# Kernel optimization log

Hardware: AMD Instinct MI355X
Metric: run time of the kernel (lower is better)

Reference implementation:

```python
import jax, jax.numpy as jnp
import numpy as np

S = 128           # seq_len
B = 256           # input_bits (bits per token, also neurons per head)
H = 16            # num_heads
NB = 12           # n_bits_per_neuron -> LUT size 2^12
PB = 7            # relative-position bits = ceil(log2(max_seq_len))
HEAD_IN = 2 * B + PB   # concat(query, key, rel_pos_bits) = 519
THRESH = H // 2


def setup_inputs() -> dict:
    key = jax.random.key(0)
    k1, k2, k3 = jax.random.split(key, 3)
    tokens = jax.random.randint(k1, (S, B), 0, 2, dtype=jnp.int32)           # binary token bits
    memory = jax.random.normal(k2, (H, B, 2 ** NB), dtype=jnp.float32)       # RAM LUT contents per head/neuron
    connections = jax.random.randint(k3, (H, B, NB), 0, HEAD_IN, dtype=jnp.int32)  # per-neuron input-bit wiring
    return {"tokens": tokens, "memory": memory, "connections": connections}


def reference(tokens, memory, connections):
    idx = jnp.arange(S)
    rel = idx[:, None] - idx[None, :]                         # [S,S] i - j
    mask = (rel >= 0).astype(jnp.int32)                        # causal mask (j <= i)
    relc = jnp.clip(rel, 0, S - 1)
    # relative-distance binary encoding, LSB first: [S,S,PB]
    pos_bits = ((relc[..., None] >> jnp.arange(PB)) & 1).astype(jnp.int32)
    q = jnp.broadcast_to(tokens[:, None, :], (S, S, B))
    k = jnp.broadcast_to(tokens[None, :, :], (S, S, B))
    head_in = jnp.concatenate([q, k, pos_bits], axis=-1)       # [S,S,HEAD_IN]
    # RAM address per (query i, key j, head h, neuron n): pack NB wired bits, LSB first
    addr = jnp.zeros((S, S, H, B), dtype=jnp.int32)
    for b in range(NB):  # tiny fixed loop over bit planes, fully vectorized over S,S,H,B
        addr = addr + (head_in[..., connections[:, :, b]] << b)
    # LUT gather: memory[h, n, addr] -> [S,S,H,B]
    h_idx = jnp.arange(H)[:, None]
    n_idx = jnp.arange(B)[None, :]
    vals = memory[h_idx, n_idx, addr]
    bits = (vals > 0.0).astype(jnp.int32)                      # RAM neuron output bit
    # XOR accumulation over attended keys == masked sum mod 2: [S,H,B]
    head_res = jnp.sum(bits * mask[:, :, None, None], axis=1) % 2
    # majority vote across heads per bit
    ones_count = jnp.sum(head_res, axis=1)                     # [S,B]
    return (ones_count > THRESH).astype(jnp.int32)
```

## Files before the change

### kernel.cpp

```cpp
#include <hip/hip_runtime.h>


#define S 128
#define B 256
#define H 16
#define NB 12

__device__ __forceinline__ unsigned sig(unsigned x) {
    return x ^ ((x >> 3) & 0x70u) ^ ((x >> 6) & 0x70u);
}

#define TW(c) ((((c) & 3) << 1) + ((c) >> 7))
#define TP(c) (((c) >> 2) & 31)

__global__ __launch_bounds__(256) void pack_kernel(
    const int* __restrict__ tokens,
    unsigned* __restrict__ tokP)
{
    const int wid  = threadIdx.x >> 6;
    const int lane = threadIdx.x & 63;
    const int4* tp = (const int4*)tokens;
    #pragma unroll
    for (int r = 0; r < 4; ++r) {
        int i = blockIdx.x * 16 + wid * 4 + r;
        int4 x = tp[i * 64 + lane];
        unsigned long long B0 = __ballot((x.x & 1) != 0);
        unsigned long long B1 = __ballot((x.y & 1) != 0);
        unsigned long long B2 = __ballot((x.z & 1) != 0);
        unsigned long long B3 = __ballot((x.w & 1) != 0);
        int c = lane >> 1;
        unsigned long long s01 = (c & 1) ? B1 : B0;
        unsigned long long s23 = (c & 1) ? B3 : B2;
        unsigned long long s   = (c & 2) ? s23 : s01;
        unsigned word = (lane & 1) ? (unsigned)(s >> 32) : (unsigned)s;
        if (lane < 8) tokP[lane * 128 + i] = word;
    }
}

__global__ __launch_bounds__(256, 4) void softram_kernel(
    const unsigned* __restrict__ tokP,
    const float* __restrict__ memory,
    const int* __restrict__ connections,
    unsigned char* __restrict__ pc)
{
    const int bid  = blockIdx.x;
    const int g    = bid >> 8;
    const int n    = bid & 255;
    const int tid  = threadIdx.x;
    const int wid  = tid >> 6;
    const int hg   = g * 4 + wid;
    const int lane = tid & 63;

    __shared__ __align__(16) unsigned char  bytetab[4 * 4096];
    __shared__ __align__(16) unsigned int   tokT[8 * S];
    __shared__ __align__(16) unsigned short akT[4][S];
    __shared__ __align__(16) unsigned short apt[4][S];
    __shared__ int            conns[4][NB];
    __shared__ unsigned int   parts[4][4];

    const float4* mrow = (const float4*)(memory + ((size_t)(hg * 256 + n) << 12));
    float4 va[16];
    #pragma unroll
    for (int t = 0; t < 16; ++t) va[t] = mrow[lane + 64 * t];

    ((int4*)tokT)[tid] = ((const int4*)tokP)[tid];
    if (tid < 4 * NB) {
        int hh = tid / NB, b = tid - hh * NB;
        conns[hh][b] = connections[(size_t)(g * 4 + hh) * (B * NB) + n * NB + b];
    }
    __syncthreads();

    unsigned qmask = 0, kmask = 0, pmask = 0;
    #pragma unroll
    for (int b = 0; b < NB; ++b) {
        int c = conns[wid][b];
        qmask |= (unsigned)(c < 256) << b;
        kmask |= (unsigned)(c >= 256 && c < 512) << b;
        pmask |= (unsigned)(c >= 512) << b;
    }
    const int qb = __popc(qmask);
    const int kb = __popc(kmask);

    unsigned char* __restrict__ bt = &bytetab[wid << 12];
    unsigned long long rlo = 0, rhi = 0;

    if (pmask == 0) {
        unsigned qclsA = 0, qclsB = 0;
        #pragma unroll
        for (int e = 0; e < 2; ++e) {
            int ii = lane + 64 * e;
            unsigned qc = 0, kc = 0;
            int qn = 0, kn = 0;
            #pragma unroll
            for (int b = 0; b < NB; ++b) {
                int c = conns[wid][b];
                if (c < 256) {
                    qc |= ((tokT[TW(c) * S + ii] >> TP(c)) & 1u) << qn;
                    ++qn;
                } else {
                    int c2 = c - 256;
                    kc |= ((tokT[TW(c2) * S + ii] >> TP(c2)) & 1u) << kn;
                    ++kn;
                }
            }
            akT[wid][ii] = (unsigned short)kc;
            if (e == 0) qclsA = qc; else qclsB = qc;
        }

        #pragma unroll
        for (int t = 0; t < 16; ++t) {
            float4 v = va[t];
            unsigned p = 4u * (unsigned)(lane + 64 * t);
            unsigned w = (unsigned)(v.x > 0.f)
                       | ((unsigned)(v.y > 0.f) << 8)
                       | ((unsigned)(v.z > 0.f) << 16)
                       | ((unsigned)(v.w > 0.f) << 24);
            *(unsigned*)&bt[sig(p)] = w;
        }

        const bool formA = (qb <= 6);
        const int SBITS  = formA ? qb : kb;
        unsigned apl = 0, aul = 0;
        {
            int scnt = 0, lcnt = 0;
            #pragma unroll
            for (int b = 0; b < NB; ++b) {
                int c = conns[wid][b];
                bool isS = formA ? (c < 256) : (c >= 256);
                if (isS) {
                    apl |= (((unsigned)lane >> scnt) & 1u) << b;
                    ++scnt;
                } else {
                    int p = SBITS + lcnt;
                    if (p < 6) apl |= (((unsigned)lane >> p) & 1u) << b;
                    else       aul |= (((unsigned)lane >> (p - 6)) & 1u) << b;
                    ++lcnt;
                }
            }
        }
        const unsigned spl  = sig(apl);
        const unsigned saul = sig(aul);
        unsigned Wlo = 0, Whi = 0;
        #pragma unroll 8
        for (int it = 0; it < 64; ++it) {
            unsigned sau  = (unsigned)__builtin_amdgcn_readlane((int)saul, it);
            unsigned bitv = bt[sau ^ spl] & 1u;
            unsigned long long Bm = __ballot(bitv != 0u);
#if __has_builtin(__builtin_amdgcn_writelane)
            Wlo = (unsigned)__builtin_amdgcn_writelane((int)(unsigned)Bm, it, (int)Wlo);
            Whi = (unsigned)__builtin_amdgcn_writelane((int)(unsigned)(Bm >> 32), it, (int)Whi);
#else
            Wlo = (lane == it) ? (unsigned)Bm : Wlo;
            Whi = (lane == it) ? (unsigned)(Bm >> 32) : Whi;
#endif
        }
        const unsigned long long Wfull = ((unsigned long long)Whi << 32) | Wlo;

        if (formA) {
            unsigned kclsA = akT[wid][lane];
            unsigned g0 = kclsA << qb;
            unsigned long long V = __shfl(Wfull, (int)(g0 >> 6)) >> (g0 & 63u);
            #pragma unroll
            for (int d = 1; d < 64; d <<= 1) {
                unsigned long long u = __shfl_up(V, (unsigned)d);
                V ^= (lane >= d) ? u : 0ull;
            }
            rlo = __ballot(((V >> qclsA) & 1ull) != 0ull);
            const unsigned long long Abase = __shfl(V, 63);

            unsigned kclsB = akT[wid][64 + lane];
            unsigned g1 = kclsB << qb;
            unsigned long long V1 = __shfl(Wfull, (int)(g1 >> 6)) >> (g1 & 63u);
            #pragma unroll
            for (int d = 1; d < 64; d <<= 1) {
                unsigned long long u = __shfl_up(V1, (unsigned)d);
                V1 ^= (lane >= d) ? u : 0ull;
            }
            V1 ^= Abase;
            rhi = __ballot(((V1 >> qclsB) & 1ull) != 0ull);
        } else {
            unsigned kclsA = akT[wid][lane];
            unsigned C = 1u << kclsA;
            #pragma unroll
            for (int d = 1; d < 64; d <<= 1) {
                unsigned u = __shfl_up(C, (unsigned)d);
                C ^= (lane >= d) ? u : 0u;
            }
            unsigned g0a = qclsA << kb;
            unsigned W0 = (unsigned)(__shfl(Wfull, (int)(g0a >> 6)) >> (g0a & 63u));
            rlo = __ballot((__popc(W0 & C) & 1) != 0);
            const unsigned Cbase = __shfl(C, 63);

            unsigned kclsB = akT[wid][64 + lane];
            unsigned C1 = 1u << kclsB;
            #pragma unroll
            for (int d = 1; d < 64; d <<= 1) {
                unsigned u = __shfl_up(C1, (unsigned)d);
                C1 ^= (lane >= d) ? u : 0u;
            }
            C1 ^= Cbase;
            unsigned g0b = qclsB << kb;
            unsigned W1 = (unsigned)(__shfl(Wfull, (int)(g0b >> 6)) >> (g0b & 63u));
            rhi = __ballot((__popc(W1 & C1) & 1) != 0);
        }
    } else {
        unsigned aqv0 = 0, aqv1 = 0;
        #pragma unroll
        for (int e = 0; e < 2; ++e) {
            int ii = lane + 64 * e;
            unsigned aq = 0, ak = 0, ap = 0;
            #pragma unroll
            for (int b = 0; b < NB; ++b) {
                int c = conns[wid][b];
                if (c < 256) {
                    aq |= ((tokT[TW(c) * S + ii] >> TP(c)) & 1u) << b;
                } else if (c < 512) {
                    int c2 = c - 256;
                    ak |= ((tokT[TW(c2) * S + ii] >> TP(c2)) & 1u) << b;
                } else {
                    ap |= (((unsigned)ii >> (c - 512)) & 1u) << b;
                }
            }
            akT[wid][ii] = (unsigned short)sig(ak);
            apt[wid][ii] = (unsigned short)sig(ap);
            if (e == 0) aqv0 = sig(aq); else aqv1 = sig(aq);
        }

        #pragma unroll
        for (int t = 0; t < 16; ++t) {
            float4 v = va[t];
            unsigned p = 4u * (unsigned)(lane + 64 * t);
            unsigned w = (unsigned)(v.x > 0.f)
                       | ((unsigned)(v.y > 0.f) << 8)
                       | ((unsigned)(v.z > 0.f) << 16)
                       | ((unsigned)(v.w > 0.f) << 24);
            *(unsigned*)&bt[sig(p)] = w;
        }

        unsigned acc0 = 0, acc1 = 0;
        for (int s8 = 0; s8 < 8; ++s8) {
            uint4 uk = *(const uint4*)&akT[wid][s8 * 8];
            #pragma unroll
            for (int t = 0; t < 8; ++t) {
                int j = s8 * 8 + t;
                unsigned w = ((const unsigned*)&uk)[t >> 1];
                unsigned akv = (w >> ((t & 1) * 16)) & 0xffffu;
                int d0 = lane - j;
                unsigned v0 = bt[aqv0 ^ akv ^ (unsigned)apt[wid][d0 & 127]] & 1u;
                acc0 ^= (d0 >= 0) ? v0 : 0u;
                int d1 = lane + 64 - j;
                unsigned v1 = bt[aqv1 ^ akv ^ (unsigned)apt[wid][d1]] & 1u;
                acc1 ^= v1;
            }
        }
        for (int s8 = 8; s8 < 16; ++s8) {
            uint4 uk = *(const uint4*)&akT[wid][s8 * 8];
            #pragma unroll
            for (int t = 0; t < 8; ++t) {
                int j = s8 * 8 + t;
                unsigned w = ((const unsigned*)&uk)[t >> 1];
                unsigned akv = (w >> ((t & 1) * 16)) & 0xffffu;
                int d1 = lane + 64 - j;
                unsigned v1 = bt[aqv1 ^ akv ^ (unsigned)apt[wid][d1 & 127]] & 1u;
                acc1 ^= (d1 >= 0) ? v1 : 0u;
            }
        }
        rlo = __ballot(acc0 != 0u);
        rhi = __ballot(acc1 != 0u);
    }

    if (lane == 0) {
        parts[wid][0] = (unsigned)rlo;
        parts[wid][1] = (unsigned)(rlo >> 32);
        parts[wid][2] = (unsigned)rhi;
        parts[wid][3] = (unsigned)(rhi >> 32);
    }
    __syncthreads();

    if (tid < S) {
        int i = tid, tot = 0;
        #pragma unroll
        for (int hh = 0; hh < 4; ++hh)
            tot += (parts[hh][i >> 5] >> (i & 31)) & 1;
        pc[((size_t)g * 256 + n) * 128 + i] = (unsigned char)tot;
    }
}

__global__ __launch_bounds__(128) void vote_kernel(
    const unsigned char* __restrict__ pc,
    int* __restrict__ out)
{
    const int n = blockIdx.x;
    const int i = threadIdx.x;
    int tot = pc[(size_t)(0 * 256 + n) * 128 + i]
            + pc[(size_t)(1 * 256 + n) * 128 + i]
            + pc[(size_t)(2 * 256 + n) * 128 + i]
            + pc[(size_t)(3 * 256 + n) * 128 + i];
    out[i * B + n] = (tot > (H / 2)) ? 1 : 0;
}

extern "C" void kernel_launch(void* const* d_in, const int* in_sizes, int n_in,
                              void* d_out, int out_size, void* d_ws, size_t ws_size,
                              hipStream_t stream) {
    const int*   tokens      = (const int*)d_in[0];
    const float* memory      = (const float*)d_in[1];
    const int*   connections = (const int*)d_in[2];
    int*         out         = (int*)d_out;
    unsigned char* pc        = (unsigned char*)d_ws;
    unsigned*      tokP      = (unsigned*)((char*)d_ws + 4 * 256 * 128);
    (void)in_sizes; (void)n_in; (void)out_size; (void)ws_size;

    pack_kernel<<<8, 256, 0, stream>>>(tokens, tokP);
    softram_kernel<<<4 * B, 256, 0, stream>>>(tokP, memory, connections, pc);
    vote_kernel<<<B, 128, 0, stream>>>(pc, out);
}
```

Measured before the change: 110.0 us.

## Stream LUT rows through LDS with async global_load_lds pipeline

Replaces the 16 register-held float4 loads of each neuron's LUT row with direct global-to-LDS async loads into a 4-slot staging ring, consumed step by step with explicit vmcnt waits. Each step refills its slot four chunks ahead. The address computation for both branches is moved ahead of the staging loop so it overlaps the memory latency. The aim is to cut VGPR pressure (64 registers for va) and raise occupancy while keeping loads in flight. In exchange it uses 16KB more LDS per block, which may itself limit occupancy, and relies on hand-written waitcnt ordering.

After: 110.4 us. About the same (+0.4%).

```diff
diff --git a/kernel.cpp b/kernel.cpp
--- a/kernel.cpp
+++ b/kernel.cpp
@@ -52,16 +52,16 @@
     const int lane = tid & 63;
 
     __shared__ __align__(16) unsigned char  bytetab[4 * 4096];
+    __shared__ __align__(16) float          stage[4][4 * 256];
     __shared__ __align__(16) unsigned int   tokT[8 * S];
     __shared__ __align__(16) unsigned short akT[4][S];
     __shared__ __align__(16) unsigned short apt[4][S];
     __shared__ int            conns[4][NB];
     __shared__ unsigned int   parts[4][4];
 
-    const float4* mrow = (const float4*)(memory + ((size_t)(hg * 256 + n) << 12));
-    float4 va[16];
-    #pragma unroll
-    for (int t = 0; t < 16; ++t) va[t] = mrow[lane + 64 * t];
+    const float* gbase = memory + ((size_t)(hg * 256 + n) << 12);
+    float*       sbase = &stage[wid][0];
+    unsigned char* __restrict__ bt = &bytetab[wid << 12];
 
     ((int4*)tokT)[tid] = ((const int4*)tokP)[tid];
     if (tid < 4 * NB) {
@@ -69,6 +69,16 @@
         conns[hh][b] = connections[(size_t)(g * 4 + hh) * (B * NB) + n * NB + b];
     }
     __syncthreads();
+
+#if __has_builtin(__builtin_amdgcn_global_load_lds)
+#define GLLD(T) __builtin_amdgcn_global_load_lds( \
+        (const __attribute__((address_space(1))) void*)(gbase + (T) * 256 + lane * 4), \
+        (__attribute__((address_space(3))) void*)(sbase + ((T) & 3) * 256), 16, 0, 0)
+#else
+#define GLLD(T) do { *(float4*)(sbase + ((T) & 3) * 256 + lane * 4) = \
+        *(const float4*)(gbase + (T) * 256 + lane * 4); } while (0)
+#endif
+    GLLD(0); GLLD(1); GLLD(2); GLLD(3);
 
     unsigned qmask = 0, kmask = 0, pmask = 0;
     #pragma unroll
@@ -80,12 +90,10 @@
     }
     const int qb = __popc(qmask);
     const int kb = __popc(kmask);
-
-    unsigned char* __restrict__ bt = &bytetab[wid << 12];
-    unsigned long long rlo = 0, rhi = 0;
-
-    if (pmask == 0) {
-        unsigned qclsA = 0, qclsB = 0;
+    const bool fast = (pmask == 0);
+
+    unsigned qclsA = 0, qclsB = 0;
+    if (fast) {
         #pragma unroll
         for (int e = 0; e < 2; ++e) {
             int ii = lane + 64 * e;
@@ -106,18 +114,52 @@
             akT[wid][ii] = (unsigned short)kc;
             if (e == 0) qclsA = qc; else qclsB = qc;
         }
-
+    } else {
         #pragma unroll
-        for (int t = 0; t < 16; ++t) {
-            float4 v = va[t];
-            unsigned p = 4u * (unsigned)(lane + 64 * t);
-            unsigned w = (unsigned)(v.x > 0.f)
-                       | ((unsigned)(v.y > 0.f) << 8)
-                       | ((unsigned)(v.z > 0.f) << 16)
-                       | ((unsigned)(v.w > 0.f) << 24);
-            *(unsigned*)&bt[sig(p)] = w;
-        }
-
+        for (int e = 0; e < 2; ++e) {
+            int ii = lane + 64 * e;
+            unsigned aq = 0, ak = 0, ap = 0;
+            #pragma unroll
+            for (int b = 0; b < NB; ++b) {
+                int c = conns[wid][b];
+                if (c < 256) {
+                    aq |= ((tokT[TW(c) * S + ii] >> TP(c)) & 1u) << b;
+                } else if (c < 512) {
+                    int c2 = c - 256;
+                    ak |= ((tokT[TW(c2) * S + ii] >> TP(c2)) & 1u) << b;
+                } else {
+                    ap |= (((unsigned)ii >> (c - 512)) & 1u) << b;
+                }
+            }
+            akT[wid][ii] = (unsigned short)sig(ak);
+            apt[wid][ii] = (unsigned short)sig(ap);
+            if (e == 0) qclsA = sig(aq); else qclsB = sig(aq);
+        }
+    }
+
+#define STEP(T, NW) do { \
+    asm volatile("s_waitcnt vmcnt(" #NW ")" ::: "memory"); \
+    __builtin_amdgcn_sched_barrier(0); \
+    float4 v = *(const float4*)(sbase + ((T) & 3) * 256 + lane * 4); \
+    unsigned w = (unsigned)(v.x > 0.f) \
+               | ((unsigned)(v.y > 0.f) << 8) \
+               | ((unsigned)(v.z > 0.f) << 16) \
+               | ((unsigned)(v.w > 0.f) << 24); \
+    asm volatile("s_waitcnt lgkmcnt(0)" ::: "memory"); \
+    __builtin_amdgcn_sched_barrier(0); \
+    if ((T) + 4 < 16) { GLLD((T) + 4); } \
+    *(unsigned*)&bt[sig(4u * (unsigned)(lane + 64 * (T)))] = w; \
+} while (0)
+
+    STEP(0, 3);  STEP(1, 3);  STEP(2, 3);  STEP(3, 3);
+    STEP(4, 3);  STEP(5, 3);  STEP(6, 3);  STEP(7, 3);
+    STEP(8, 3);  STEP(9, 3);  STEP(10, 3); STEP(11, 3);
+    STEP(12, 3); STEP(13, 2); STEP(14, 1); STEP(15, 0);
+#undef STEP
+
+    unsigned long long rlo = 0, rhi = 0;
+
+    if (fast) {
         const bool formA = (qb <= 6);
         const int SBITS  = formA ? qb : kb;
         unsigned apl = 0, aul = 0;
@@ -204,39 +246,7 @@
             rhi = __ballot((__popc(W1 & C1) & 1) != 0);
         }
     } else {
-        unsigned aqv0 = 0, aqv1 = 0;
-        #pragma unroll
-        for (int e = 0; e < 2; ++e) {
-            int ii = lane + 64 * e;
-            unsigned aq = 0, ak = 0, ap = 0;
-            #pragma unroll
-            for (int b = 0; b < NB; ++b) {
-                int c = conns[wid][b];
-                if (c < 256) {
-                    aq |= ((tokT[TW(c) * S + ii] >> TP(c)) & 1u) << b;
-                } else if (c < 512) {
-                    int c2 = c - 256;
-                    ak |= ((tokT[TW(c2) * S + ii] >> TP(c2)) & 1u) << b;
-                } else {
-                    ap |= (((unsigned)ii >> (c - 512)) & 1u) << b;
-                }
-            }
-            akT[wid][ii] = (unsigned short)sig(ak);
-            apt[wid][ii] = (unsigned short)sig(ap);
-            if (e == 0) aqv0 = sig(aq); else aqv1 = sig(aq);
-        }
-
-        #pragma unroll
-        for (int t = 0; t < 16; ++t) {
-            float4 v = va[t];
-            unsigned p = 4u * (unsigned)(lane + 64 * t);
-            unsigned w = (unsigned)(v.x > 0.f)
-                       | ((unsigned)(v.y > 0.f) << 8)
-                       | ((unsigned)(v.z > 0.f) << 16)
-                       | ((unsigned)(v.w > 0.f) << 24);
-            *(unsigned*)&bt[sig(p)] = w;
-        }
-
+        const unsigned aqv0 = qclsA, aqv1 = qclsB;
         unsigned acc0 = 0, acc1 = 0;
         for (int s8 = 0; s8 < 8; ++s8) {
             uint4 uk = *(const uint4*)&akT[wid][s8 * 8];
```

## Move LUT thresholding and W-matrix construction into a separate prep kernel

Applied to the files above, without the earlier changes.

Splits the work so a new prep kernel reads the float LUT memory, thresholds it into a byte table, and for neurons with no position bits also builds the 64x64 bit matrix W, which goes to workspace. The main kernel then loads either the precomputed W (fast path) or the precomputed byte table, the latter via global-to-LDS loads. The goal is to take the large memory read and 16-float4 register array out of the main kernel to ease register pressure and shorten its critical path. In exchange it adds an extra global write/read round trip through workspace (up to 16 MB of byte tables), though the memory read itself is spread over more blocks.

After: 118.0 us. 7.3% more time.

```diff
diff --git a/kernel.cpp b/kernel.cpp
--- a/kernel.cpp
+++ b/kernel.cpp
@@ -13,34 +13,119 @@
 #define TW(c) ((((c) & 3) << 1) + ((c) >> 7))
 #define TP(c) (((c) >> 2) & 31)
 
-__global__ __launch_bounds__(256) void pack_kernel(
+__global__ __launch_bounds__(256, 4) void prep_kernel(
     const int* __restrict__ tokens,
-    unsigned* __restrict__ tokP)
+    const float* __restrict__ memory,
+    const int* __restrict__ connections,
+    unsigned* __restrict__ tokP,
+    unsigned long long* __restrict__ psW,
+    unsigned char* __restrict__ psB)
 {
     const int wid  = threadIdx.x >> 6;
     const int lane = threadIdx.x & 63;
-    const int4* tp = (const int4*)tokens;
+
+    if (blockIdx.x >= 1024) {
+        const int bid2 = blockIdx.x - 1024;
+        const int4* tp = (const int4*)tokens;
+        #pragma unroll
+        for (int rr = 0; rr < 4; ++rr) {
+            int i = bid2 * 16 + wid * 4 + rr;
+            int4 x = tp[i * 64 + lane];
+            unsigned long long B0 = __ballot((x.x & 1) != 0);
+            unsigned long long B1 = __ballot((x.y & 1) != 0);
+            unsigned long long B2 = __ballot((x.z & 1) != 0);
+            unsigned long long B3 = __ballot((x.w & 1) != 0);
+            int c = lane >> 1;
+            unsigned long long s01 = (c & 1) ? B1 : B0;
+            unsigned long long s23 = (c & 1) ? B3 : B2;
+            unsigned long long s   = (c & 2) ? s23 : s01;
+            unsigned word = (lane & 1) ? (unsigned)(s >> 32) : (unsigned)s;
+            if (lane < 8) tokP[lane * 128 + i] = word;
+        }
+        return;
+    }
+
+    __shared__ __align__(16) unsigned char bytetab[4][4096];
+    const int r = blockIdx.x * 4 + wid;
+    unsigned char* __restrict__ bt = bytetab[wid];
+
+    int c_l = (lane < NB) ? connections[(size_t)r * NB + lane] : 0;
+    unsigned qmask = 0, kmask = 0, pmask = 0;
     #pragma unroll
-    for (int r = 0; r < 4; ++r) {
-        int i = blockIdx.x * 16 + wid * 4 + r;
-        int4 x = tp[i * 64 + lane];
-        unsigned long long B0 = __ballot((x.x & 1) != 0);
-        unsigned long long B1 = __ballot((x.y & 1) != 0);
-        unsigned long long B2 = __ballot((x.z & 1) != 0);
-        unsigned long long B3 = __ballot((x.w & 1) != 0);
-        int c = lane >> 1;
-        unsigned long long s01 = (c & 1) ? B1 : B0;
-        unsigned long long s23 = (c & 1) ? B3 : B2;
-        unsigned long long s   = (c & 2) ? s23 : s01;
-        unsigned word = (lane & 1) ? (unsigned)(s >> 32) : (unsigned)s;
-        if (lane < 8) tokP[lane * 128 + i] = word;
-    }
+    for (int b = 0; b < NB; ++b) {
+        int cb = __shfl(c_l, b);
+        qmask |= (unsigned)(cb < 256) << b;
+        kmask |= (unsigned)(cb >= 256 && cb < 512) << b;
+        pmask |= (unsigned)(cb >= 512) << b;
+    }
+    const int qb = __popc(qmask);
+    const int kb = __popc(kmask);
+    const bool fast = (pmask == 0);
+
+    const float4* mp = (const float4*)(memory + ((size_t)r << 12));
+    unsigned char* __restrict__ gb = psB + ((size_t)r << 12);
+    float4 va[4];
+    #pragma unroll
+    for (int t = 0; t < 4; ++t) va[t] = mp[lane + 64 * t];
+    #pragma unroll
+    for (int t = 0; t < 16; ++t) {
+        float4 v = va[t & 3];
+        if (t + 4 < 16) va[t & 3] = mp[lane + 64 * (t + 4)];
+        unsigned w = (unsigned)(v.x > 0.f)
+                   | ((unsigned)(v.y > 0.f) << 8)
+                   | ((unsigned)(v.z > 0.f) << 16)
+                   | ((unsigned)(v.w > 0.f) << 24);
+        unsigned sp = sig(4u * (unsigned)(lane + 64 * t));
+        *(unsigned*)&bt[sp] = w;
+        if (!fast) *(unsigned*)&gb[sp] = w;
+    }
+
+    if (!fast) return;
+
+    const bool formA = (qb <= 6);
+    const int SBITS  = formA ? qb : kb;
+    unsigned apl = 0, aul = 0;
+    {
+        int scnt = 0, lcnt = 0;
+        #pragma unroll
+        for (int b = 0; b < NB; ++b) {
+            int cb = __shfl(c_l, b);
+            bool isS = formA ? (cb < 256) : (cb >= 256);
+            if (isS) {
+                apl |= (((unsigned)lane >> scnt) & 1u) << b;
+                ++scnt;
+            } else {
+                int p = SBITS + lcnt;
+                if (p < 6) apl |= (((unsigned)lane >> p) & 1u) << b;
+                else       aul |= (((unsigned)lane >> (p - 6)) & 1u) << b;
+                ++lcnt;
+            }
+        }
+    }
+    const unsigned spl  = sig(apl);
+    const unsigned saul = sig(aul);
+    unsigned Wlo = 0, Whi = 0;
+    #pragma unroll 8
+    for (int it = 0; it < 64; ++it) {
+        unsigned sau  = (unsigned)__builtin_amdgcn_readlane((int)saul, it);
+        unsigned bitv = bt[sau ^ spl] & 1u;
+        unsigned long long Bm = __ballot(bitv != 0u);
+#if __has_builtin(__builtin_amdgcn_writelane)
+        Wlo = (unsigned)__builtin_amdgcn_writelane((int)(unsigned)Bm, it, (int)Wlo);
+        Whi = (unsigned)__builtin_amdgcn_writelane((int)(unsigned)(Bm >> 32), it, (int)Whi);
+#else
+        Wlo = (lane == it) ? (unsigned)Bm : Wlo;
+        Whi = (lane == it) ? (unsigned)(Bm >> 32) : Whi;
+#endif
+    }
+    psW[(size_t)r * 64 + lane] = ((unsigned long long)Whi << 32) | Wlo;
 }
 
 __global__ __launch_bounds__(256, 4) void softram_kernel(
     const unsigned* __restrict__ tokP,
-    const float* __restrict__ memory,
     const int* __restrict__ connections,
+    const unsigned long long* __restrict__ psW,
+    const unsigned char* __restrict__ psB,
     unsigned char* __restrict__ pc)
 {
     const int bid  = blockIdx.x;
@@ -49,19 +134,17 @@
     const int tid  = threadIdx.x;
     const int wid  = tid >> 6;
     const int hg   = g * 4 + wid;
+    const int r    = hg * 256 + n;
     const int lane = tid & 63;
 
-    __shared__ __align__(16) unsigned char  bytetab[4 * 4096];
+    __shared__ __align__(16) unsigned char  bytetab[4][4096];
     __shared__ __align__(16) unsigned int   tokT[8 * S];
     __shared__ __align__(16) unsigned short akT[4][S];
     __shared__ __align__(16) unsigned short apt[4][S];
     __shared__ int            conns[4][NB];
     __shared__ unsigned int   parts[4][4];
 
-    const float4* mrow = (const float4*)(memory + ((size_t)(hg * 256 + n) << 12));
-    float4 va[16];
-    #pragma unroll
-    for (int t = 0; t < 16; ++t) va[t] = mrow[lane + 64 * t];
+    unsigned char* __restrict__ bt = bytetab[wid];
 
     ((int4*)tokT)[tid] = ((const int4*)tokP)[tid];
     if (tid < 4 * NB) {
@@ -80,11 +163,13 @@
     }
     const int qb = __popc(qmask);
     const int kb = __popc(kmask);
-
-    unsigned char* __restrict__ bt = &bytetab[wid << 12];
+    const bool fast = (pmask == 0);
+
     unsigned long long rlo = 0, rhi = 0;
 
-    if (pmask == 0) {
+    if (fast) {
+        const unsigned long long Wfull = psW[(size_t)r * 64 + lane];
+
         unsigned qclsA = 0, qclsB = 0;
         #pragma unroll
         for (int e = 0; e < 2; ++e) {
@@ -107,56 +192,7 @@
             if (e == 0) qclsA = qc; else qclsB = qc;
         }
 
-        #pragma unroll
-        for (int t = 0; t < 16; ++t) {
-            float4 v = va[t];
-            unsigned p = 4u * (unsigned)(lane + 64 * t);
-            unsigned w = (unsigned)(v.x > 0.f)
-                       | ((unsigned)(v.y > 0.f) << 8)
-                       | ((unsigned)(v.z > 0.f) << 16)
-                       | ((unsigned)(v.w > 0.f) << 24);
-            *(unsigned*)&bt[sig(p)] = w;
-        }
-
-        const bool formA = (qb <= 6);
-        const int SBITS  = formA ? qb : kb;
-        unsigned apl = 0, aul = 0;
-        {
-            int scnt = 0, lcnt = 0;
-            #pragma unroll
-            for (int b = 0; b < NB; ++b) {
-                int c = conns[wid][b];
-                bool isS = formA ? (c < 256) : (c >= 256);
-                if (isS) {
-                    apl |= (((unsigned)lane >> scnt) & 1u) << b;
-                    ++scnt;
-                } else {
-                    int p = SBITS + lcnt;
-                    if (p < 6) apl |= (((unsigned)lane >> p) & 1u) << b;
-                    else       aul |= (((unsigned)lane >> (p - 6)) & 1u) << b;
-                    ++lcnt;
-                }
-            }
-        }
-        const unsigned spl  = sig(apl);
-        const unsigned saul = sig(aul);
-        unsigned Wlo = 0, Whi = 0;
-        #pragma unroll 8
-        for (int it = 0; it < 64; ++it) {
-            unsigned sau  = (unsigned)__builtin_amdgcn_readlane((int)saul, it);
-            unsigned bitv = bt[sau ^ spl] & 1u;
-            unsigned long long Bm = __ballot(bitv != 0u);
-#if __has_builtin(__builtin_amdgcn_writelane)
-            Wlo = (unsigned)__builtin_amdgcn_writelane((int)(unsigned)Bm, it, (int)Wlo);
-            Whi = (unsigned)__builtin_amdgcn_writelane((int)(unsigned)(Bm >> 32), it, (int)Whi);
-#else
-            Wlo = (lane == it) ? (unsigned)Bm : Wlo;
-            Whi = (lane == it) ? (unsigned)(Bm >> 32) : Whi;
-#endif
-        }
-        const unsigned long long Wfull = ((unsigned long long)Whi << 32) | Wlo;
-
-        if (formA) {
+        if (qb <= 6) {
             unsigned kclsA = akT[wid][lane];
             unsigned g0 = kclsA << qb;
             unsigned long long V = __shfl(Wfull, (int)(g0 >> 6)) >> (g0 & 63u);
@@ -204,6 +240,21 @@
             rhi = __ballot((__popc(W1 & C1) & 1) != 0);
         }
     } else {
+        const unsigned char* __restrict__ gb = psB + ((size_t)r << 12);
+#if __has_builtin(__builtin_amdgcn_global_load_lds)
+        #pragma unroll
+        for (int t = 0; t < 4; ++t)
+            __builtin_amdgcn_global_load_lds(
+                (const __attribute__((address_space(1))) void*)(gb + t * 1024 + lane * 16),
+                (__attribute__((address_space(3))) void*)(bt + t * 1024 + lane * 16),
+                16, 0, 0);
+#else
+        #pragma unroll
+        for (int t = 0; t < 4; ++t)
+            *(float4*)(bt + t * 1024 + lane * 16) =
+                *(const float4*)(gb + t * 1024 + lane * 16);
+#endif
+
         unsigned aqv0 = 0, aqv1 = 0;
         #pragma unroll
         for (int e = 0; e < 2; ++e) {
@@ -226,16 +277,8 @@
             if (e == 0) aqv0 = sig(aq); else aqv1 = sig(aq);
         }
 
-        #pragma unroll
-        for (int t = 0; t < 16; ++t) {
-            float4 v = va[t];
-            unsigned p = 4u * (unsigned)(lane + 64 * t);
-            unsigned w = (unsigned)(v.x > 0.f)
-                       | ((unsigned)(v.y > 0.f) << 8)
-                       | ((unsigned)(v.z > 0.f) << 16)
-                       | ((unsigned)(v.w > 0.f) << 24);
-            *(unsigned*)&bt[sig(p)] = w;
-        }
+        asm volatile("s_waitcnt vmcnt(0)" ::: "memory");
+        __builtin_amdgcn_sched_barrier(0);
 
         unsigned acc0 = 0, acc1 = 0;
         for (int s8 = 0; s8 < 8; ++s8) {
@@ -306,11 +349,13 @@
     const float* memory      = (const float*)d_in[1];
     const int*   connections = (const int*)d_in[2];
     int*         out         = (int*)d_out;
-    unsigned char* pc        = (unsigned char*)d_ws;
-    unsigned*      tokP      = (unsigned*)((char*)d_ws + 4 * 256 * 128);
+    unsigned char*      pc   = (unsigned char*)d_ws;
+    unsigned*           tokP = (unsigned*)((char*)d_ws + (128u << 10));
+    unsigned long long* psW  = (unsigned long long*)((char*)d_ws + (1u << 20));
+    unsigned char*      psB  = (unsigned char*)d_ws + (4u << 20);
     (void)in_sizes; (void)n_in; (void)out_size; (void)ws_size;
 
-    pack_kernel<<<8, 256, 0, stream>>>(tokens, tokP);
-    softram_kernel<<<4 * B, 256, 0, stream>>>(tokP, memory, connections, pc);
+    prep_kernel<<<1032, 256, 0, stream>>>(tokens, memory, connections, tokP, psW, psB);
+    softram_kernel<<<4 * B, 256, 0, stream>>>(tokP, connections, psW, psB, pc);
     vote_kernel<<<B, 128, 0, stream>>>(pc, out);
 }
```

## Split each neuron's work across two waves and double blocks with register-light memory loads

Applied to the files above, without the earlier changes.

Each (head, neuron) row now gets two wavefronts, one per half of the query range. Each wave loads half of the LUT row, and the LUT-gather loop is split 32/32 between them. Partial results, prefix bases and fallback parity are exchanged through shared memory and extra barriers. Connections are broadcast through shuffles instead of shared memory, and the register footprint drops (va[16] becomes a rolling va[4]), which allows 8 blocks per CU. The intent is more parallelism and occupancy to hide the memory-bound LUT loads. The cost is added synchronisation and a vote kernel that now reads 16 per-head bitmasks per output.

Measured after the change: 108.3 us. About the same (-1.5%).

```diff
diff --git a/kernel.cpp b/kernel.cpp
--- a/kernel.cpp
+++ b/kernel.cpp
@@ -37,87 +37,113 @@
     }
 }
 
-__global__ __launch_bounds__(256, 4) void softram_kernel(
+__global__ __launch_bounds__(256, 8) void softram_kernel(
     const unsigned* __restrict__ tokP,
     const float* __restrict__ memory,
     const int* __restrict__ connections,
-    unsigned char* __restrict__ pc)
+    unsigned long long* __restrict__ pres)
 {
-    const int bid  = blockIdx.x;
-    const int g    = bid >> 8;
-    const int n    = bid & 255;
     const int tid  = threadIdx.x;
     const int wid  = tid >> 6;
-    const int hg   = g * 4 + wid;
+    const int rs   = wid >> 1;
+    const int sub  = wid & 1;
+    const int r    = blockIdx.x * 2 + rs;
     const int lane = tid & 63;
 
-    __shared__ __align__(16) unsigned char  bytetab[4 * 4096];
-    __shared__ __align__(16) unsigned int   tokT[8 * S];
-    __shared__ __align__(16) unsigned short akT[4][S];
-    __shared__ __align__(16) unsigned short apt[4][S];
-    __shared__ int            conns[4][NB];
-    __shared__ unsigned int   parts[4][4];
-
-    const float4* mrow = (const float4*)(memory + ((size_t)(hg * 256 + n) << 12));
-    float4 va[16];
-    #pragma unroll
-    for (int t = 0; t < 16; ++t) va[t] = mrow[lane + 64 * t];
-
-    ((int4*)tokT)[tid] = ((const int4*)tokP)[tid];
-    if (tid < 4 * NB) {
-        int hh = tid / NB, b = tid - hh * NB;
-        conns[hh][b] = connections[(size_t)(g * 4 + hh) * (B * NB) + n * NB + b];
-    }
-    __syncthreads();
+    __shared__ __align__(16) unsigned char      bytetab[2][4096];
+    __shared__ __align__(16) unsigned int       tokT[8 * S];
+    __shared__ __align__(16) unsigned short     akT[2][S];
+    __shared__ __align__(16) unsigned short     apt[2][S];
+    __shared__ __align__(16) unsigned short     aqs[2][S];
+    __shared__ __align__(16) unsigned long long wsh[2][64];
+    __shared__ unsigned long long baseS[2];
+    __shared__ unsigned long long fbu[2];
+
+    unsigned char* __restrict__ bt = bytetab[rs];
+
+    const float4* mp = (const float4*)(memory + ((size_t)r << 12));
+    float4 va[4];
+    #pragma unroll
+    for (int t = 0; t < 4; ++t) va[t] = mp[lane + 64 * (sub * 8 + t)];
+
+    int c_l = (lane < NB) ? connections[(size_t)r * NB + lane] : 0;
+    int cb[NB];
+    #pragma unroll
+    for (int b = 0; b < NB; ++b)
+        cb[b] = __builtin_amdgcn_readfirstlane(__shfl(c_l, b));
 
     unsigned qmask = 0, kmask = 0, pmask = 0;
     #pragma unroll
     for (int b = 0; b < NB; ++b) {
-        int c = conns[wid][b];
-        qmask |= (unsigned)(c < 256) << b;
-        kmask |= (unsigned)(c >= 256 && c < 512) << b;
-        pmask |= (unsigned)(c >= 512) << b;
+        qmask |= (unsigned)(cb[b] < 256) << b;
+        kmask |= (unsigned)(cb[b] >= 256 && cb[b] < 512) << b;
+        pmask |= (unsigned)(cb[b] >= 512) << b;
     }
     const int qb = __popc(qmask);
     const int kb = __popc(kmask);
-
-    unsigned char* __restrict__ bt = &bytetab[wid << 12];
-    unsigned long long rlo = 0, rhi = 0;
-
-    if (pmask == 0) {
-        unsigned qclsA = 0, qclsB = 0;
+    const bool fast = (pmask == 0);
+
+    ((int4*)tokT)[tid] = ((const int4*)tokP)[tid];
+    __syncthreads();
+
+    const int ii = sub * 64 + lane;
+    unsigned qcls = 0;
+    if (fast) {
+        unsigned qc = 0, kc = 0;
+        int qn = 0, kn = 0;
         #pragma unroll
-        for (int e = 0; e < 2; ++e) {
-            int ii = lane + 64 * e;
-            unsigned qc = 0, kc = 0;
-            int qn = 0, kn = 0;
-            #pragma unroll
-            for (int b = 0; b < NB; ++b) {
-                int c = conns[wid][b];
-                if (c < 256) {
-                    qc |= ((tokT[TW(c) * S + ii] >> TP(c)) & 1u) << qn;
-                    ++qn;
-                } else {
-                    int c2 = c - 256;
-                    kc |= ((tokT[TW(c2) * S + ii] >> TP(c2)) & 1u) << kn;
-                    ++kn;
-                }
-            }
-            akT[wid][ii] = (unsigned short)kc;
-            if (e == 0) qclsA = qc; else qclsB = qc;
-        }
-
+        for (int b = 0; b < NB; ++b) {
+            int c = cb[b];
+            if (c < 256) {
+                qc |= ((tokT[TW(c) * S + ii] >> TP(c)) & 1u) << qn;
+                ++qn;
+            } else {
+                int c2 = c - 256;
+                kc |= ((tokT[TW(c2) * S + ii] >> TP(c2)) & 1u) << kn;
+                ++kn;
+            }
+        }
+        akT[rs][ii] = (unsigned short)kc;
+        qcls = qc;
+    } else {
+        unsigned aq = 0, ak = 0, ap = 0;
         #pragma unroll
-        for (int t = 0; t < 16; ++t) {
-            float4 v = va[t];
-            unsigned p = 4u * (unsigned)(lane + 64 * t);
-            unsigned w = (unsigned)(v.x > 0.f)
-                       | ((unsigned)(v.y > 0.f) << 8)
-                       | ((unsigned)(v.z > 0.f) << 16)
-                       | ((unsigned)(v.w > 0.f) << 24);
-            *(unsigned*)&bt[sig(p)] = w;
-        }
-
+        for (int b = 0; b < NB; ++b) {
+            int c = cb[b];
+            if (c < 256) {
+                aq |= ((tokT[TW(c) * S + ii] >> TP(c)) & 1u) << b;
+            } else if (c < 512) {
+                int c2 = c - 256;
+                ak |= ((tokT[TW(c2) * S + ii] >> TP(c2)) & 1u) << b;
+            } else {
+                ap |= (((unsigned)ii >> (c - 512)) & 1u) << b;
+            }
+        }
+        akT[rs][ii] = (unsigned short)sig(ak);
+        apt[rs][ii] = (unsigned short)sig(ap);
+        aqs[rs][ii] = (unsigned short)sig(aq);
+        qcls = sig(aq);
+    }
+
+    #pragma unroll
+    for (int t = 0; t < 8; ++t) {
+        float4 v = va[t & 3];
+        if (t + 4 < 8) va[t & 3] = mp[lane + 64 * (sub * 8 + t + 4)];
+        unsigned w = (unsigned)(v.x > 0.f)
+                   | ((unsigned)(v.y > 0.f) << 8)
+                   | ((unsigned)(v.z > 0.f) << 16)
+                   | ((unsigned)(v.w > 0.f) << 24);
+        *(unsigned*)&bt[sig(4u * (unsigned)(lane + 64 * (sub * 8 + t)))] = w;
+    }
+    __syncthreads();
+
+    unsigned long long rpart = 0;
+    unsigned long long Wfull = 0;
+    unsigned long long Vreg  = 0;
+    unsigned Creg = 0;
+    unsigned acc_fb = 0;
+
+    if (fast) {
         const bool formA = (qb <= 6);
         const int SBITS  = formA ? qb : kb;
         unsigned apl = 0, aul = 0;
@@ -125,7 +151,7 @@
             int scnt = 0, lcnt = 0;
             #pragma unroll
             for (int b = 0; b < NB; ++b) {
-                int c = conns[wid][b];
+                int c = cb[b];
                 bool isS = formA ? (c < 256) : (c >= 256);
                 if (isS) {
                     apl |= (((unsigned)lane >> scnt) & 1u) << b;
@@ -142,160 +168,130 @@
         const unsigned saul = sig(aul);
         unsigned Wlo = 0, Whi = 0;
         #pragma unroll 8
-        for (int it = 0; it < 64; ++it) {
+        for (int k = 0; k < 32; ++k) {
+            int it = sub * 32 + k;
             unsigned sau  = (unsigned)__builtin_amdgcn_readlane((int)saul, it);
             unsigned bitv = bt[sau ^ spl] & 1u;
             unsigned long long Bm = __ballot(bitv != 0u);
-#if __has_builtin(__builtin_amdgcn_writelane)
-            Wlo = (unsigned)__builtin_amdgcn_writelane((int)(unsigned)Bm, it, (int)Wlo);
-            Whi = (unsigned)__builtin_amdgcn_writelane((int)(unsigned)(Bm >> 32), it, (int)Whi);
-#else
             Wlo = (lane == it) ? (unsigned)Bm : Wlo;
             Whi = (lane == it) ? (unsigned)(Bm >> 32) : Whi;
-#endif
-        }
-        const unsigned long long Wfull = ((unsigned long long)Whi << 32) | Wlo;
-
+        }
+        if ((lane >> 5) == sub)
+            wsh[rs][lane] = ((unsigned long long)Whi << 32) | Wlo;
+    } else {
+        if (sub == 0) {
+            const unsigned aqv0 = qcls;
+            const unsigned aqvU = aqs[rs][64 + lane];
+            unsigned acc0 = 0, accP = 0;
+            for (int s8 = 0; s8 < 8; ++s8) {
+                uint4 uk = *(const uint4*)&akT[rs][s8 * 8];
+                #pragma unroll
+                for (int t = 0; t < 8; ++t) {
+                    int j = s8 * 8 + t;
+                    unsigned w = ((const unsigned*)&uk)[t >> 1];
+                    unsigned akv = (w >> ((t & 1) * 16)) & 0xffffu;
+                    int d0 = lane - j;
+                    unsigned v0 = bt[aqv0 ^ akv ^ (unsigned)apt[rs][d0 & 127]] & 1u;
+                    acc0 ^= (d0 >= 0) ? v0 : 0u;
+                    int d1 = lane + 64 - j;
+                    unsigned v1 = bt[aqvU ^ akv ^ (unsigned)apt[rs][d1]] & 1u;
+                    accP ^= v1;
+                }
+            }
+            rpart = __ballot(acc0 != 0u);
+            unsigned long long up = __ballot(accP != 0u);
+            if (lane == 0) fbu[rs] = up;
+        } else {
+            const unsigned aqv1 = qcls;
+            unsigned acc1 = 0;
+            for (int s8 = 8; s8 < 16; ++s8) {
+                uint4 uk = *(const uint4*)&akT[rs][s8 * 8];
+                #pragma unroll
+                for (int t = 0; t < 8; ++t) {
+                    int j = s8 * 8 + t;
+                    unsigned w = ((const unsigned*)&uk)[t >> 1];
+                    unsigned akv = (w >> ((t & 1) * 16)) & 0xffffu;
+                    int d1 = lane + 64 - j;
+                    unsigned v1 = bt[aqv1 ^ akv ^ (unsigned)apt[rs][d1 & 127]] & 1u;
+                    acc1 ^= (d1 >= 0) ? v1 : 0u;
+                }
+            }
+            acc_fb = acc1;
+        }
+    }
+    __syncthreads();
+
+    if (fast) {
+        Wfull = wsh[rs][lane];
+        const bool formA = (qb <= 6);
         if (formA) {
-            unsigned kclsA = akT[wid][lane];
-            unsigned g0 = kclsA << qb;
+            unsigned kcls = akT[rs][ii];
+            unsigned g0 = kcls << qb;
             unsigned long long V = __shfl(Wfull, (int)(g0 >> 6)) >> (g0 & 63u);
             #pragma unroll
             for (int d = 1; d < 64; d <<= 1) {
                 unsigned long long u = __shfl_up(V, (unsigned)d);
                 V ^= (lane >= d) ? u : 0ull;
             }
-            rlo = __ballot(((V >> qclsA) & 1ull) != 0ull);
-            const unsigned long long Abase = __shfl(V, 63);
-
-            unsigned kclsB = akT[wid][64 + lane];
-            unsigned g1 = kclsB << qb;
-            unsigned long long V1 = __shfl(Wfull, (int)(g1 >> 6)) >> (g1 & 63u);
-            #pragma unroll
-            for (int d = 1; d < 64; d <<= 1) {
-                unsigned long long u = __shfl_up(V1, (unsigned)d);
-                V1 ^= (lane >= d) ? u : 0ull;
-            }
-            V1 ^= Abase;
-            rhi = __ballot(((V1 >> qclsB) & 1ull) != 0ull);
+            if (sub == 0) {
+                rpart = __ballot(((V >> qcls) & 1ull) != 0ull);
+                unsigned long long Ab = __shfl(V, 63);
+                if (lane == 0) baseS[rs] = Ab;
+            } else {
+                Vreg = V;
+            }
         } else {
-            unsigned kclsA = akT[wid][lane];
-            unsigned C = 1u << kclsA;
+            unsigned kcls = akT[rs][ii];
+            unsigned C = 1u << kcls;
             #pragma unroll
             for (int d = 1; d < 64; d <<= 1) {
                 unsigned u = __shfl_up(C, (unsigned)d);
                 C ^= (lane >= d) ? u : 0u;
             }
-            unsigned g0a = qclsA << kb;
-            unsigned W0 = (unsigned)(__shfl(Wfull, (int)(g0a >> 6)) >> (g0a & 63u));
-            rlo = __ballot((__popc(W0 & C) & 1) != 0);
-            const unsigned Cbase = __shfl(C, 63);
-
-            unsigned kclsB = akT[wid][64 + lane];
-            unsigned C1 = 1u << kclsB;
-            #pragma unroll
-            for (int d = 1; d < 64; d <<= 1) {
-                unsigned u = __shfl_up(C1, (unsigned)d);
-                C1 ^= (lane >= d) ? u : 0u;
-            }
-            C1 ^= Cbase;
-            unsigned g0b = qclsB << kb;
+            if (sub == 0) {
+                unsigned g0a = qcls << kb;
+                unsigned W0 = (unsigned)(__shfl(Wfull, (int)(g0a >> 6)) >> (g0a & 63u));
+                rpart = __ballot((__popc(W0 & C) & 1) != 0);
+                unsigned Cb = __shfl(C, 63);
+                if (lane == 0) baseS[rs] = (unsigned long long)Cb;
+            } else {
+                Creg = C;
+            }
+        }
+    } else if (sub == 1) {
+        unsigned long long up = fbu[rs];
+        acc_fb ^= (unsigned)((up >> lane) & 1ull);
+        rpart = __ballot(acc_fb != 0u);
+    }
+    __syncthreads();
+
+    if (fast && sub == 1) {
+        const bool formA = (qb <= 6);
+        if (formA) {
+            unsigned long long V1 = Vreg ^ baseS[rs];
+            rpart = __ballot(((V1 >> qcls) & 1ull) != 0ull);
+        } else {
+            unsigned C1 = Creg ^ (unsigned)baseS[rs];
+            unsigned g0b = qcls << kb;
             unsigned W1 = (unsigned)(__shfl(Wfull, (int)(g0b >> 6)) >> (g0b & 63u));
-            rhi = __ballot((__popc(W1 & C1) & 1) != 0);
-        }
-    } else {
-        unsigned aqv0 = 0, aqv1 = 0;
-        #pragma unroll
-        for (int e = 0; e < 2; ++e) {
-            int ii = lane + 64 * e;
-            unsigned aq = 0, ak = 0, ap = 0;
-            #pragma unroll
-            for (int b = 0; b < NB; ++b) {
-                int c = conns[wid][b];
-                if (c < 256) {
-                    aq |= ((tokT[TW(c) * S + ii] >> TP(c)) & 1u) << b;
-                } else if (c < 512) {
-                    int c2 = c - 256;
-                    ak |= ((tokT[TW(c2) * S + ii] >> TP(c2)) & 1u) << b;
-                } else {
-                    ap |= (((unsigned)ii >> (c - 512)) & 1u) << b;
-                }
-            }
-            akT[wid][ii] = (unsigned short)sig(ak);
-            apt[wid][ii] = (unsigned short)sig(ap);
-            if (e == 0) aqv0 = sig(aq); else aqv1 = sig(aq);
-        }
-
-        #pragma unroll
-        for (int t = 0; t < 16; ++t) {
-            float4 v = va[t];
-            unsigned p = 4u * (unsigned)(lane + 64 * t);
-            unsigned w = (unsigned)(v.x > 0.f)
-                       | ((unsigned)(v.y > 0.f) << 8)
-                       | ((unsigned)(v.z > 0.f) << 16)
-                       | ((unsigned)(v.w > 0.f) << 24);
-            *(unsigned*)&bt[sig(p)] = w;
-        }
-
-        unsigned acc0 = 0, acc1 = 0;
-        for (int s8 = 0; s8 < 8; ++s8) {
-            uint4 uk = *(const uint4*)&akT[wid][s8 * 8];
-            #pragma unroll
-            for (int t = 0; t < 8; ++t) {
-                int j = s8 * 8 + t;
-                unsigned w = ((const unsigned*)&uk)[t >> 1];
-                unsigned akv = (w >> ((t & 1) * 16)) & 0xffffu;
-                int d0 = lane - j;
-                unsigned v0 = bt[aqv0 ^ akv ^ (unsigned)apt[wid][d0 & 127]] & 1u;
-                acc0 ^= (d0 >= 0) ? v0 : 0u;
-                int d1 = lane + 64 - j;
-                unsigned v1 = bt[aqv1 ^ akv ^ (unsigned)apt[wid][d1]] & 1u;
-                acc1 ^= v1;
-            }
-        }
-        for (int s8 = 8; s8 < 16; ++s8) {
-            uint4 uk = *(const uint4*)&akT[wid][s8 * 8];
-            #pragma unroll
-            for (int t = 0; t < 8; ++t) {
-                int j = s8 * 8 + t;
-                unsigned w = ((const unsigned*)&uk)[t >> 1];
-                unsigned akv = (w >> ((t & 1) * 16)) & 0xffffu;
-                int d1 = lane + 64 - j;
-                unsigned v1 = bt[aqv1 ^ akv ^ (unsigned)apt[wid][d1 & 127]] & 1u;
-                acc1 ^= (d1 >= 0) ? v1 : 0u;
-            }
-        }
-        rlo = __ballot(acc0 != 0u);
-        rhi = __ballot(acc1 != 0u);
-    }
-
-    if (lane == 0) {
-        parts[wid][0] = (unsigned)rlo;
-        parts[wid][1] = (unsigned)(rlo >> 32);
-        parts[wid][2] = (unsigned)rhi;
-        parts[wid][3] = (unsigned)(rhi >> 32);
-    }
-    __syncthreads();
-
-    if (tid < S) {
-        int i = tid, tot = 0;
-        #pragma unroll
-        for (int hh = 0; hh < 4; ++hh)
-            tot += (parts[hh][i >> 5] >> (i & 31)) & 1;
-        pc[((size_t)g * 256 + n) * 128 + i] = (unsigned char)tot;
-    }
+            rpart = __ballot((__popc(W1 & C1) & 1) != 0);
+        }
+    }
+
+    if (lane == 0) pres[(size_t)r * 2 + sub] = rpart;
 }
 
 __global__ __launch_bounds__(128) void vote_kernel(
-    const unsigned char* __restrict__ pc,
+    const unsigned long long* __restrict__ pres,
     int* __restrict__ out)
 {
     const int n = blockIdx.x;
     const int i = threadIdx.x;
-    int tot = pc[(size_t)(0 * 256 + n) * 128 + i]
-            + pc[(size_t)(1 * 256 + n) * 128 + i]
-            + pc[(size_t)(2 * 256 + n) * 128 + i]
-            + pc[(size_t)(3 * 256 + n) * 128 + i];
+    const int w = i >> 6, b = i & 63;
+    int tot = 0;
+    #pragma unroll
+    for (int h = 0; h < H; ++h)
+        tot += (int)((pres[(size_t)(h * 256 + n) * 2 + w] >> b) & 1ull);
     out[i * B + n] = (tot > (H / 2)) ? 1 : 0;
 }
 
@@ -306,11 +302,11 @@
     const float* memory      = (const float*)d_in[1];
     const int*   connections = (const int*)d_in[2];
     int*         out         = (int*)d_out;
-    unsigned char* pc        = (unsigned char*)d_ws;
-    unsigned*      tokP      = (unsigned*)((char*)d_ws + 4 * 256 * 128);
+    unsigned long long* pres = (unsigned long long*)d_ws;
+    unsigned*           tokP = (unsigned*)((char*)d_ws + (64u << 10));
     (void)in_sizes; (void)n_in; (void)out_size; (void)ws_size;
 
     pack_kernel<<<8, 256, 0, stream>>>(tokens, tokP);
-    softram_kernel<<<4 * B, 256, 0, stream>>>(tokP, memory, connections, pc);
-    vote_kernel<<<B, 128, 0, stream>>>(pc, out);
-}
+    softram_kernel<<<2048, 256, 0, stream>>>(tokP, memory, connections, pres);
+    vote_kernel<<<B, 128, 0, stream>>>(pres, out);
+}
```
